# Performance work log

Measured on AMD Instinct MI355X. Metric: run time of the kernel, lower is better.

The kernel has to match this reference:

```python
import jax, jax.numpy as jnp
import numpy as np

H = 16  # n_heads


def setup_inputs() -> dict:
    key = jax.random.key(0)
    ks = jax.random.split(key, 11)
    B, S, D = 2, 2048, 1024
    def rn(k, shape, scale=1.0):
        return jax.random.normal(k, shape, dtype=jnp.float32) * scale
    w_scale = 1.0 / np.sqrt(D)
    return {
        "queries": rn(ks[0], (B, S, D)),
        "keys": rn(ks[1], (B, S, D)),
        "values": rn(ks[2], (B, S, D)),
        "Wq": rn(ks[3], (D, D), w_scale), "bq": rn(ks[4], (D,), 0.02),
        "Wk": rn(ks[5], (D, D), w_scale), "bk": rn(ks[6], (D,), 0.02),
        "Wv": rn(ks[7], (D, D), w_scale), "bv": rn(ks[8], (D,), 0.02),
        "Wo": rn(ks[9], (D, D), w_scale), "bo": rn(ks[10], (D,), 0.02),
    }


def _split_heads(x, h):
    # [B, S, D] -> [B, h, S, D/h]
    B, S, D = x.shape
    return x.reshape(B, S, h, D // h).transpose(0, 2, 1, 3)


def reference(queries, keys, values, Wq, bq, Wk, bk, Wv, bv, Wo, bo):
    B, S, D = queries.shape
    Q = _split_heads(queries @ Wq + bq, H)  # [B,h,S,dk]
    K = _split_heads(keys @ Wk + bk, H)
    V = _split_heads(values @ Wv + bv, H)
    # Faithful quirk: scale by sqrt(seq_len), not sqrt(d_k)
    factor = jnp.sqrt(jnp.asarray(S, dtype=Q.dtype))
    scores = jnp.einsum("bhqd,bhkd->bhqk", Q, K) / factor  # [B,h,S,S]
    weights = jax.nn.softmax(scores, axis=-1)
    attn = jnp.einsum("bhqk,bhkd->bhqd", weights, V)  # [B,h,S,dk]
    attn = attn.transpose(0, 2, 1, 3).reshape(B, S, D)  # [B,S,D]
    return attn @ Wo + bo
```

## Files before the change

kernel.cpp:

```cpp
#include <hip/hip_runtime.h>

typedef unsigned short ushort_t;
typedef unsigned int uint_t;
typedef __attribute__((ext_vector_type(8))) short short8;
typedef __attribute__((ext_vector_type(4))) float floatx4;

#define QSCALE 0.03187936f

__device__ __forceinline__ ushort_t f2bf(float f) {
    union { float f; uint_t u; } c; c.f = f;
    uint_t u = c.u;
    return (ushort_t)((u + 0x7fffu + ((u >> 16) & 1u)) >> 16);
}
__device__ __forceinline__ floatx4 mfma16x32(short8 a, short8 b, floatx4 c) {
    return __builtin_amdgcn_mfma_f32_16x16x32_bf16(a, b, c, 0, 0, 0);
}
__device__ __forceinline__ floatx4 zero4() { floatx4 z = {0.f, 0.f, 0.f, 0.f}; return z; }

__device__ __forceinline__ void gload16(const ushort_t* g, ushort_t* l) {
    __builtin_amdgcn_global_load_lds(
        (const __attribute__((address_space(1))) void*)g,
        (__attribute__((address_space(3))) void*)l, 16, 0, 0);
}

__global__ __launch_bounds__(256) void cvt_bf16(
    const float* __restrict__ s0, const float* __restrict__ s1,
    const float* __restrict__ s2, ushort_t* __restrict__ d0,
    ushort_t* __restrict__ d1, ushort_t* __restrict__ d2)
{
    const int which = blockIdx.x >> 11;
    const int blk = blockIdx.x & 2047;
    const float* src = (which == 0) ? s0 : (which == 1) ? s1 : s2;
    ushort_t* dst = (which == 0) ? d0 : (which == 1) ? d1 : d2;
    const int i = (blk * 256 + threadIdx.x) * 8;
    float4 f0 = *(const float4*)(src + i);
    float4 f1 = *(const float4*)(src + i + 4);
    __align__(16) ushort_t t[8];
    t[0] = f2bf(f0.x); t[1] = f2bf(f0.y); t[2] = f2bf(f0.z); t[3] = f2bf(f0.w);
    t[4] = f2bf(f1.x); t[5] = f2bf(f1.y); t[6] = f2bf(f1.z); t[7] = f2bf(f1.w);
    *(uint4*)(dst + i) = *(uint4*)t;
}

__global__ __launch_bounds__(256) void transpose_w(
    const float* __restrict__ W0, const float* __restrict__ W1,
    const float* __restrict__ W2, const float* __restrict__ W3,
    ushort_t* __restrict__ WT)
{
    __shared__ ushort_t tile[64][65];
    const float* W = (blockIdx.y == 0) ? W0 : (blockIdx.y == 1) ? W1
                   : (blockIdx.y == 2) ? W2 : W3;
    ushort_t* dst = WT + (size_t)blockIdx.y * (1024 * 1024);
    const int t = threadIdx.x;
    const int r = t >> 2, p = t & 3;
    const int j0 = (blockIdx.x & 15) << 6, k0 = (blockIdx.x >> 4) << 6;

    const float* src = W + (size_t)(k0 + r) * 1024 + j0 + p * 16;
    float4 f0 = *(const float4*)(src);
    float4 f1 = *(const float4*)(src + 4);
    float4 f2 = *(const float4*)(src + 8);
    float4 f3 = *(const float4*)(src + 12);
    ushort_t* tr = &tile[r][p * 16];
    tr[0] = f2bf(f0.x); tr[1] = f2bf(f0.y); tr[2]  = f2bf(f0.z); tr[3]  = f2bf(f0.w);
    tr[4] = f2bf(f1.x); tr[5] = f2bf(f1.y); tr[6]  = f2bf(f1.z); tr[7]  = f2bf(f1.w);
    tr[8] = f2bf(f2.x); tr[9] = f2bf(f2.y); tr[10] = f2bf(f2.z); tr[11] = f2bf(f2.w);
    tr[12] = f2bf(f3.x); tr[13] = f2bf(f3.y); tr[14] = f2bf(f3.z); tr[15] = f2bf(f3.w);
    __syncthreads();
    __align__(16) ushort_t buf[16];
#pragma unroll
    for (int i = 0; i < 16; ++i) buf[i] = tile[p * 16 + i][r];
    ushort_t* o = dst + (size_t)(j0 + r) * 1024 + k0 + p * 16;
    *(uint4*)(o)     = *(uint4*)(buf);
    *(uint4*)(o + 8) = *(uint4*)(buf + 8);
}

__global__ __launch_bounds__(256) void gemm_bt(
    const ushort_t* __restrict__ A0, const ushort_t* __restrict__ A1,
    const ushort_t* __restrict__ A2, const ushort_t* __restrict__ WT,
    const float* __restrict__ b0, const float* __restrict__ b1,
    const float* __restrict__ b2,
    ushort_t* __restrict__ Dq, ushort_t* __restrict__ Dk,
    ushort_t* __restrict__ Dv, int zbase)
{
    __shared__ __align__(16) ushort_t As[128 * 32];
    __shared__ __align__(16) ushort_t Bs[128 * 32];

    const int mode = blockIdx.z + zbase;
    const ushort_t* A = (mode == 0) ? A0 : (mode == 1) ? A1 : A2;
    const float* bias = (mode == 0) ? b0 : (mode == 1) ? b1 : b2;
    const ushort_t* Bt = WT + (size_t)mode * 1048576;

    const int tid = threadIdx.x;
    const int lane = tid & 63, wid = tid >> 6;
    const int quad = lane >> 4, l16 = lane & 15;
    const int wm = wid >> 1, wn = wid & 1;
    const int row0 = blockIdx.y << 7, col0 = blockIdx.x << 7;

    floatx4 acc[4][4];
#pragma unroll
    for (int i = 0; i < 4; ++i)
#pragma unroll
        for (int j = 0; j < 4; ++j) acc[i][j] = zero4();

    const int i0 = tid, i1 = 256 + tid;
    const int r0_ = i0 >> 2, c0_ = (i0 & 3) ^ (r0_ & 3);
    const int r1_ = i1 >> 2, c1_ = (i1 & 3) ^ (r1_ & 3);
    const ushort_t* gA0 = A  + (size_t)(row0 + r0_) * 1024 + c0_ * 8;
    const ushort_t* gA1 = A  + (size_t)(row0 + r1_) * 1024 + c1_ * 8;
    const ushort_t* gB0 = Bt + (size_t)(col0 + r0_) * 1024 + c0_ * 8;
    const ushort_t* gB1 = Bt + (size_t)(col0 + r1_) * 1024 + c1_ * 8;
    ushort_t* lA0 = As + i0 * 8;  ushort_t* lA1 = As + i1 * 8;
    ushort_t* lB0 = Bs + i0 * 8;  ushort_t* lB1 = Bs + i1 * 8;

    const int ra = wm * 64 + l16, rb = wn * 64 + l16;
    const int sa_off = (quad ^ (l16 & 3)) * 8;

    for (int k0 = 0; k0 < 1024; k0 += 32) {
        __syncthreads();
        gload16(gA0 + k0, lA0);
        gload16(gA1 + k0, lA1);
        gload16(gB0 + k0, lB0);
        gload16(gB1 + k0, lB1);
        __syncthreads();

        short8 af[4], bf[4];
#pragma unroll
        for (int i = 0; i < 4; ++i)
            af[i] = *(const short8*)(As + (ra + i * 16) * 32 + sa_off);
#pragma unroll
        for (int j = 0; j < 4; ++j)
            bf[j] = *(const short8*)(Bs + (rb + j * 16) * 32 + sa_off);
#pragma unroll
        for (int i = 0; i < 4; ++i)
#pragma unroll
            for (int j = 0; j < 4; ++j)
                acc[i][j] = mfma16x32(af[i], bf[j], acc[i][j]);
    }

    const float sc = (mode == 0) ? QSCALE : 1.f;
#pragma unroll
    for (int i = 0; i < 4; ++i) {
#pragma unroll
        for (int j = 0; j < 4; ++j) {
            const int c = col0 + wn * 64 + j * 16 + l16;
            const float bv = bias[c];
#pragma unroll
            for (int rr = 0; rr < 4; ++rr) {
                const int r = row0 + wm * 64 + i * 16 + quad * 4 + rr;
                const float v = (acc[i][j][rr] + bv) * sc;
                const int b = r >> 11, s = r & 2047, h = c >> 6, d = c & 63;
                if (mode <= 1) {
                    ushort_t* D = (mode == 0) ? Dq : Dk;
                    D[(((b * 16 + h) * 2048 + s) << 6) + d] = f2bf(v);
                } else {
                    Dv[(((b * 16 + h) * 64 + d) << 11) + s] = f2bf(v);
                }
            }
        }
    }
}

__global__ __launch_bounds__(256) void gemm64(
    const ushort_t* __restrict__ A, const ushort_t* __restrict__ Bt,
    const float* __restrict__ bias, float* __restrict__ Dout)
{
    __shared__ __align__(16) ushort_t As[64 * 32];
    __shared__ __align__(16) ushort_t Bs[128 * 32];
    const int tid = threadIdx.x;
    const int lane = tid & 63, wid = tid >> 6;
    const int quad = lane >> 4, l16 = lane & 15;
    const int wm = wid >> 1, wn = wid & 1;
    const int row0 = blockIdx.y << 6, col0 = blockIdx.x << 7;

    floatx4 acc[2][4];
#pragma unroll
    for (int i = 0; i < 2; ++i)
#pragma unroll
        for (int j = 0; j < 4; ++j) acc[i][j] = zero4();

    const int rA = tid >> 2, cA = (tid & 3) ^ (rA & 3);
    const ushort_t* gA = A + (size_t)(row0 + rA) * 1024 + cA * 8;
    ushort_t* lA = As + tid * 8;
    const int i0 = tid, i1 = 256 + tid;
    const int rB0 = i0 >> 2, cB0 = (i0 & 3) ^ (rB0 & 3);
    const int rB1 = i1 >> 2, cB1 = (i1 & 3) ^ (rB1 & 3);
    const ushort_t* gB0 = Bt + (size_t)(col0 + rB0) * 1024 + cB0 * 8;
    const ushort_t* gB1 = Bt + (size_t)(col0 + rB1) * 1024 + cB1 * 8;
    ushort_t* lB0 = Bs + i0 * 8;  ushort_t* lB1 = Bs + i1 * 8;

    const int sa_off = (quad ^ (l16 & 3)) * 8;

    for (int k0 = 0; k0 < 1024; k0 += 32) {
        __syncthreads();
        gload16(gA + k0, lA);
        gload16(gB0 + k0, lB0);
        gload16(gB1 + k0, lB1);
        __syncthreads();

        short8 af[2], bf[4];
#pragma unroll
        for (int i = 0; i < 2; ++i)
            af[i] = *(const short8*)(As + (wm * 32 + i * 16 + l16) * 32 + sa_off);
#pragma unroll
        for (int j = 0; j < 4; ++j)
            bf[j] = *(const short8*)(Bs + (wn * 64 + j * 16 + l16) * 32 + sa_off);
#pragma unroll
        for (int i = 0; i < 2; ++i)
#pragma unroll
            for (int j = 0; j < 4; ++j)
                acc[i][j] = mfma16x32(af[i], bf[j], acc[i][j]);
    }

#pragma unroll
    for (int i = 0; i < 2; ++i)
#pragma unroll
        for (int j = 0; j < 4; ++j) {
            const int c = col0 + wn * 64 + j * 16 + l16;
            const float bv = bias[c];
#pragma unroll
            for (int rr = 0; rr < 4; ++rr) {
                const int r = row0 + wm * 32 + i * 16 + quad * 4 + rr;
                Dout[(size_t)r * 1024 + c] = acc[i][j][rr] + bv;
            }
        }
}

__global__ __launch_bounds__(256, 4) void attn64(
    const ushort_t* __restrict__ Q, const ushort_t* __restrict__ K,
    const ushort_t* __restrict__ Vt, ushort_t* __restrict__ Out)
{
    __shared__ __align__(16) ushort_t Ks[64 * 64];
    __shared__ __align__(16) ushort_t Vs[64 * 64];

    const int tid = threadIdx.x;
    const int lane = tid & 63, wid = tid >> 6;
    const int quad = lane >> 4, l16 = lane & 15;
    const int blk = blockIdx.x;
    const int bh = blk & 31;
    const int q0 = (blk >> 5) << 6;

    const ushort_t* Qh = Q + (size_t)bh * (2048 * 64);
    const ushort_t* Kh = K + (size_t)bh * (2048 * 64);
    const ushort_t* Vh = Vt + (size_t)bh * (64 * 2048);

    const int qr = q0 + wid * 16 + l16;
    const short8 qf0 = *(const short8*)(Qh + (size_t)qr * 64 + quad * 8);
    const short8 qf1 = *(const short8*)(Qh + (size_t)qr * 64 + 32 + quad * 8);

    float l_st = 0.f;
    floatx4 o_acc[4];
#pragma unroll
    for (int d = 0; d < 4; ++d) o_acc[d] = zero4();

    const int i0 = tid, i1 = 256 + tid;
    const int kr0 = i0 >> 3, kc0 = (i0 & 7) ^ (kr0 & 7);
    const int kr1 = i1 >> 3, kc1 = (i1 & 7) ^ (kr1 & 7);
    const ushort_t* gK0 = Kh + (size_t)kr0 * 64 + kc0 * 8;
    const ushort_t* gK1 = Kh + (size_t)kr1 * 64 + kc1 * 8;
    const ushort_t* gV0 = Vh + (size_t)kr0 * 2048 + kc0 * 8;
    const ushort_t* gV1 = Vh + (size_t)kr1 * 2048 + kc1 * 8;
    ushort_t* lK0 = Ks + i0 * 8;  ushort_t* lK1 = Ks + i1 * 8;
    ushort_t* lV0 = Vs + i0 * 8;  ushort_t* lV1 = Vs + i1 * 8;

    const int l7 = l16 & 7;
    const int q2 = quad >> 1, q1 = (quad & 1) * 4;

    for (int kt = 0; kt < 2048; kt += 64) {
        __syncthreads();
        gload16(gK0 + (size_t)kt * 64, lK0);
        gload16(gK1 + (size_t)kt * 64, lK1);
        gload16(gV0 + kt, lV0);
        gload16(gV1 + kt, lV1);
        __syncthreads();

        floatx4 sa[4];
#pragma unroll
        for (int g = 0; g < 4; ++g) {
            const int row = g * 16 + l16;
            const short8 kf0 = *(const short8*)(Ks + row * 64 + ((quad ^ l7) * 8));
            const short8 kf1 = *(const short8*)(Ks + row * 64 + (((quad + 4) ^ l7) * 8));
            sa[g] = mfma16x32(kf0, qf0, zero4());
            sa[g] = mfma16x32(kf1, qf1, sa[g]);
        }

#pragma unroll
        for (int G = 0; G < 2; ++G) {
            uint_t ub[8];
#pragma unroll
            for (int t = 0; t < 8; ++t) {
                const int g = G * 2 + (t >> 2), r = t & 3;
                const float e = __builtin_amdgcn_exp2f(fminf(sa[g][r], 80.f));
                const uint_t u = __float_as_uint(e) & 0xffff0000u;
                l_st += __uint_as_float(u);
                ub[t] = u;
            }
            union { uint_t u[4]; short8 s; } pc;
            pc.u[0] = (ub[0] >> 16) | ub[1];
            pc.u[1] = (ub[2] >> 16) | ub[3];
            pc.u[2] = (ub[4] >> 16) | ub[5];
            pc.u[3] = (ub[6] >> 16) | ub[7];
            const short8 pf = pc.s;

            const int ch0 = ((4 * G + q2) ^ l7) * 8;
            const int ch1 = ((4 * G + 2 + q2) ^ l7) * 8;
#pragma unroll
            for (int db = 0; db < 4; ++db) {
                const int vbase = (db * 16 + l16) * 64 + q1;
                const uint2 v0 = *(const uint2*)(Vs + vbase + ch0);
                const uint2 v1 = *(const uint2*)(Vs + vbase + ch1);
                union { uint_t u[4]; short8 s; } vc;
                vc.u[0] = v0.x; vc.u[1] = v0.y; vc.u[2] = v1.x; vc.u[3] = v1.y;
                o_acc[db] = mfma16x32(pf, vc.s, o_acc[db]);
            }
        }
    }

    l_st += __shfl_xor(l_st, 16);
    l_st += __shfl_xor(l_st, 32);

    const int b = bh >> 4, h = bh & 15;
    const int s0 = q0 + wid * 16 + quad * 4;
#pragma unroll
    for (int r = 0; r < 4; ++r) {
        const float lr = __shfl(l_st, quad * 4 + r);
        const float inv = 1.f / lr;
#pragma unroll
        for (int db = 0; db < 4; ++db) {
            const float v = o_acc[db][r] * inv;
            Out[(size_t)(b * 2048 + s0 + r) * 1024 + h * 64 + db * 16 + l16] = f2bf(v);
        }
    }
}

extern "C" void kernel_launch(void* const* d_in, const int* in_sizes, int n_in,
                              void* d_out, int out_size, void* d_ws, size_t ws_size,
                              hipStream_t stream) {
    const float* queries = (const float*)d_in[0];
    const float* keys    = (const float*)d_in[1];
    const float* values  = (const float*)d_in[2];
    const float* Wq = (const float*)d_in[3];
    const float* bq = (const float*)d_in[4];
    const float* Wk = (const float*)d_in[5];
    const float* bk = (const float*)d_in[6];
    const float* Wv = (const float*)d_in[7];
    const float* bv = (const float*)d_in[8];
    const float* Wo = (const float*)d_in[9];
    const float* bo = (const float*)d_in[10];
    float* out = (float*)d_out;

    char* ws = (char*)d_ws;
    const size_t MB = 1024 * 1024;
    ushort_t* WT = (ushort_t*)(ws);
    const ushort_t* WoT = WT + 3 * 1048576;
    dim3 tb(256);

    transpose_w<<<dim3(256, 4), tb, 0, stream>>>(Wq, Wk, Wv, Wo, WT);

    if (ws_size >= 64 * MB) {
        ushort_t* Qb  = (ushort_t*)(ws + 8 * MB);
        ushort_t* Kb  = (ushort_t*)(ws + 16 * MB);
        ushort_t* Vb  = (ushort_t*)(ws + 24 * MB);
        ushort_t* Qp  = (ushort_t*)(ws + 32 * MB);
        ushort_t* Kp  = (ushort_t*)(ws + 40 * MB);
        ushort_t* Vtp = (ushort_t*)(ws + 48 * MB);
        ushort_t* An  = (ushort_t*)(ws + 56 * MB);
        cvt_bf16<<<dim3(6144), tb, 0, stream>>>(queries, keys, values, Qb, Kb, Vb);
        gemm_bt<<<dim3(8, 32, 3), tb, 0, stream>>>(Qb, Kb, Vb, WT,
            bq, bk, bv, Qp, Kp, Vtp, 0);
        attn64<<<dim3(1024), tb, 0, stream>>>(Qp, Kp, Vtp, An);
        gemm64<<<dim3(8, 64), tb, 0, stream>>>(An, WoT, bo, out);
    } else {
        ushort_t* buf1 = (ushort_t*)(ws + 8 * MB);
        ushort_t* buf2 = (ushort_t*)(ws + 16 * MB);
        ushort_t* Qp   = (ushort_t*)(ws + 24 * MB);
        ushort_t* Kp   = (ushort_t*)(ws + 32 * MB);
        cvt_bf16<<<dim3(4096), tb, 0, stream>>>(queries, keys, keys, buf1, buf2, buf2);
        gemm_bt<<<dim3(8, 32, 2), tb, 0, stream>>>(buf1, buf2, buf2, WT,
            bq, bk, bk, Qp, Kp, Kp, 0);
        cvt_bf16<<<dim3(2048), tb, 0, stream>>>(values, values, values, buf1, buf1, buf1);
        gemm_bt<<<dim3(8, 32, 1), tb, 0, stream>>>(buf1, buf1, buf1, WT,
            bv, bv, bv, buf2, buf2, buf2, 2);
        attn64<<<dim3(1024), tb, 0, stream>>>(Qp, Kp, buf2, buf1);
        gemm64<<<dim3(8, 64), tb, 0, stream>>>(buf1, WoT, bo, out);
    }
}
```

Measured before the change: 233.2 us.

## Give each attention wave two 16-row query tiles and halve block threads

The attention kernel now runs 128-thread blocks (two waves) where each wave handles 32 query rows as two 16-row sub-tiles. Each K and V fragment read from LDS feeds two MFMAs, and each thread issues four global-to-LDS loads per K/V tile instead of two. This cuts LDS traffic and the load-instruction count per query row. In exchange each wave holds twice the accumulators and score registers, and the kernel drops from four waves to two per block, which may reduce occupancy and latency hiding.

```diff
diff --git a/kernel.cpp b/kernel.cpp
--- a/kernel.cpp
+++ b/kernel.cpp
@@ -224,7 +224,7 @@
         }
 }
 
-__global__ __launch_bounds__(256, 4) void attn64(
+__global__ __launch_bounds__(128, 2) void attn64q(
     const ushort_t* __restrict__ Q, const ushort_t* __restrict__ K,
     const ushort_t* __restrict__ Vt, ushort_t* __restrict__ Out)
 {
@@ -242,64 +242,73 @@
     const ushort_t* Kh = K + (size_t)bh * (2048 * 64);
     const ushort_t* Vh = Vt + (size_t)bh * (64 * 2048);
 
-    const int qr = q0 + wid * 16 + l16;
-    const short8 qf0 = *(const short8*)(Qh + (size_t)qr * 64 + quad * 8);
-    const short8 qf1 = *(const short8*)(Qh + (size_t)qr * 64 + 32 + quad * 8);
-
-    float l_st = 0.f;
-    floatx4 o_acc[4];
-#pragma unroll
-    for (int d = 0; d < 4; ++d) o_acc[d] = zero4();
-
-    const int i0 = tid, i1 = 256 + tid;
-    const int kr0 = i0 >> 3, kc0 = (i0 & 7) ^ (kr0 & 7);
-    const int kr1 = i1 >> 3, kc1 = (i1 & 7) ^ (kr1 & 7);
-    const ushort_t* gK0 = Kh + (size_t)kr0 * 64 + kc0 * 8;
-    const ushort_t* gK1 = Kh + (size_t)kr1 * 64 + kc1 * 8;
-    const ushort_t* gV0 = Vh + (size_t)kr0 * 2048 + kc0 * 8;
-    const ushort_t* gV1 = Vh + (size_t)kr1 * 2048 + kc1 * 8;
-    ushort_t* lK0 = Ks + i0 * 8;  ushort_t* lK1 = Ks + i1 * 8;
-    ushort_t* lV0 = Vs + i0 * 8;  ushort_t* lV1 = Vs + i1 * 8;
+    short8 qf0[2], qf1[2];
+#pragma unroll
+    for (int u = 0; u < 2; ++u) {
+        const int qr = q0 + wid * 32 + u * 16 + l16;
+        qf0[u] = *(const short8*)(Qh + (size_t)qr * 64 + quad * 8);
+        qf1[u] = *(const short8*)(Qh + (size_t)qr * 64 + 32 + quad * 8);
+    }
+
+    float l_st[2] = {0.f, 0.f};
+    floatx4 o_acc[2][4];
+#pragma unroll
+    for (int u = 0; u < 2; ++u)
+#pragma unroll
+        for (int d = 0; d < 4; ++d) o_acc[u][d] = zero4();
+
+    const int kr = tid >> 3, kc = (tid & 7) ^ (kr & 7);
+    const ushort_t* gK0 = Kh + (size_t)kr * 64 + kc * 8;
+    const ushort_t* gV0 = Vh + (size_t)kr * 2048 + kc * 8;
+    ushort_t* lK0 = Ks + tid * 8;
+    ushort_t* lV0 = Vs + tid * 8;
 
     const int l7 = l16 & 7;
     const int q2 = quad >> 1, q1 = (quad & 1) * 4;
 
     for (int kt = 0; kt < 2048; kt += 64) {
         __syncthreads();
-        gload16(gK0 + (size_t)kt * 64, lK0);
-        gload16(gK1 + (size_t)kt * 64, lK1);
-        gload16(gV0 + kt, lV0);
-        gload16(gV1 + kt, lV1);
-        __syncthreads();
-
-        floatx4 sa[4];
+#pragma unroll
+        for (int i = 0; i < 4; ++i) {
+            gload16(gK0 + (size_t)kt * 64 + i * 1024, lK0 + i * 1024);
+            gload16(gV0 + kt + (size_t)i * 32768, lV0 + i * 1024);
+        }
+        __syncthreads();
+
+        floatx4 sa[2][4];
 #pragma unroll
         for (int g = 0; g < 4; ++g) {
             const int row = g * 16 + l16;
             const short8 kf0 = *(const short8*)(Ks + row * 64 + ((quad ^ l7) * 8));
             const short8 kf1 = *(const short8*)(Ks + row * 64 + (((quad + 4) ^ l7) * 8));
-            sa[g] = mfma16x32(kf0, qf0, zero4());
-            sa[g] = mfma16x32(kf1, qf1, sa[g]);
+#pragma unroll
+            for (int u = 0; u < 2; ++u) {
+                floatx4 t0 = mfma16x32(kf0, qf0[u], zero4());
+                sa[u][g] = mfma16x32(kf1, qf1[u], t0);
+            }
         }
 
 #pragma unroll
         for (int G = 0; G < 2; ++G) {
-            uint_t ub[8];
-#pragma unroll
-            for (int t = 0; t < 8; ++t) {
-                const int g = G * 2 + (t >> 2), r = t & 3;
-                const float e = __builtin_amdgcn_exp2f(fminf(sa[g][r], 80.f));
-                const uint_t u = __float_as_uint(e) & 0xffff0000u;
-                l_st += __uint_as_float(u);
-                ub[t] = u;
-            }
-            union { uint_t u[4]; short8 s; } pc;
-            pc.u[0] = (ub[0] >> 16) | ub[1];
-            pc.u[1] = (ub[2] >> 16) | ub[3];
-            pc.u[2] = (ub[4] >> 16) | ub[5];
-            pc.u[3] = (ub[6] >> 16) | ub[7];
-            const short8 pf = pc.s;
-
+            short8 pf[2];
+#pragma unroll
+            for (int u = 0; u < 2; ++u) {
+                uint_t ub[8];
+#pragma unroll
+                for (int t = 0; t < 8; ++t) {
+                    const int g = G * 2 + (t >> 2), r = t & 3;
+                    const float e = __builtin_amdgcn_exp2f(fminf(sa[u][g][r], 80.f));
+                    const uint_t uu = __float_as_uint(e) & 0xffff0000u;
+                    l_st[u] += __uint_as_float(uu);
+                    ub[t] = uu;
+                }
+                union { uint_t u4[4]; short8 s; } pc;
+                pc.u4[0] = (ub[0] >> 16) | ub[1];
+                pc.u4[1] = (ub[2] >> 16) | ub[3];
+                pc.u4[2] = (ub[4] >> 16) | ub[5];
+                pc.u4[3] = (ub[6] >> 16) | ub[7];
+                pf[u] = pc.s;
+            }
             const int ch0 = ((4 * G + q2) ^ l7) * 8;
             const int ch1 = ((4 * G + 2 + q2) ^ l7) * 8;
 #pragma unroll
@@ -307,26 +316,30 @@
                 const int vbase = (db * 16 + l16) * 64 + q1;
                 const uint2 v0 = *(const uint2*)(Vs + vbase + ch0);
                 const uint2 v1 = *(const uint2*)(Vs + vbase + ch1);
-                union { uint_t u[4]; short8 s; } vc;
-                vc.u[0] = v0.x; vc.u[1] = v0.y; vc.u[2] = v1.x; vc.u[3] = v1.y;
-                o_acc[db] = mfma16x32(pf, vc.s, o_acc[db]);
-            }
-        }
-    }
-
-    l_st += __shfl_xor(l_st, 16);
-    l_st += __shfl_xor(l_st, 32);
-
-    const int b = bh >> 4, h = bh & 15;
-    const int s0 = q0 + wid * 16 + quad * 4;
-#pragma unroll
-    for (int r = 0; r < 4; ++r) {
-        const float lr = __shfl(l_st, quad * 4 + r);
-        const float inv = 1.f / lr;
-#pragma unroll
-        for (int db = 0; db < 4; ++db) {
-            const float v = o_acc[db][r] * inv;
-            Out[(size_t)(b * 2048 + s0 + r) * 1024 + h * 64 + db * 16 + l16] = f2bf(v);
+                union { uint_t u4[4]; short8 s; } vc;
+                vc.u4[0] = v0.x; vc.u4[1] = v0.y; vc.u4[2] = v1.x; vc.u4[3] = v1.y;
+                o_acc[0][db] = mfma16x32(pf[0], vc.s, o_acc[0][db]);
+                o_acc[1][db] = mfma16x32(pf[1], vc.s, o_acc[1][db]);
+            }
+        }
+    }
+
+    const int b = bh >> 4, hh = bh & 15;
+#pragma unroll
+    for (int u = 0; u < 2; ++u) {
+        float l = l_st[u];
+        l += __shfl_xor(l, 16);
+        l += __shfl_xor(l, 32);
+        const int s0 = q0 + wid * 32 + u * 16 + quad * 4;
+#pragma unroll
+        for (int r = 0; r < 4; ++r) {
+            const float lr = __shfl(l, quad * 4 + r);
+            const float inv = 1.f / lr;
+#pragma unroll
+            for (int db = 0; db < 4; ++db) {
+                const float v = o_acc[u][db][r] * inv;
+                Out[(size_t)(b * 2048 + s0 + r) * 1024 + hh * 64 + db * 16 + l16] = f2bf(v);
+            }
         }
     }
 }
@@ -352,6 +365,7 @@
     ushort_t* WT = (ushort_t*)(ws);
     const ushort_t* WoT = WT + 3 * 1048576;
     dim3 tb(256);
+    dim3 ta(128);
 
     transpose_w<<<dim3(256, 4), tb, 0, stream>>>(Wq, Wk, Wv, Wo, WT);
 
@@ -366,7 +380,7 @@
         cvt_bf16<<<dim3(6144), tb, 0, stream>>>(queries, keys, values, Qb, Kb, Vb);
         gemm_bt<<<dim3(8, 32, 3), tb, 0, stream>>>(Qb, Kb, Vb, WT,
             bq, bk, bv, Qp, Kp, Vtp, 0);
-        attn64<<<dim3(1024), tb, 0, stream>>>(Qp, Kp, Vtp, An);
+        attn64q<<<dim3(1024), ta, 0, stream>>>(Qp, Kp, Vtp, An);
         gemm64<<<dim3(8, 64), tb, 0, stream>>>(An, WoT, bo, out);
     } else {
         ushort_t* buf1 = (ushort_t*)(ws + 8 * MB);
@@ -379,7 +393,7 @@
         cvt_bf16<<<dim3(2048), tb, 0, stream>>>(values, values, values, buf1, buf1, buf1);
         gemm_bt<<<dim3(8, 32, 1), tb, 0, stream>>>(buf1, buf1, buf1, WT,
             bv, bv, bv, buf2, buf2, buf2, 2);
-        attn64<<<dim3(1024), tb, 0, stream>>>(Qp, Kp, buf2, buf1);
+        attn64q<<<dim3(1024), ta, 0, stream>>>(Qp, Kp, buf2, buf1);
         gemm64<<<dim3(8, 64), tb, 0, stream>>>(buf1, WoT, bo, out);
     }
 }
```

Result: slower. 241.3 us (+3.5%).
